# Kernel optimization log

Hardware: AMD Instinct MI355X
Metric: run time of the kernel (lower is better)

The kernel has to match this reference:

```python
import jax, jax.numpy as jnp
import numpy as np

EPS = 1e-07
CURVATURE = 1.0
MAX_NORM_RATIO = 0.99
B, L, N, K = 4, 2048, 2048, 2048


def _ternary_init(key, n, k):
    rand = jax.random.normal(key, (n, k), dtype=jnp.float32)
    threshold = 0.5 * jnp.mean(jnp.abs(rand))
    return jnp.where(rand > threshold, 1.0,
                     jnp.where(rand < -threshold, -1.0, 0.0)).astype(jnp.float32)


def setup_inputs() -> dict:
    key = jax.random.key(0)
    kx, kw = jax.random.split(key)
    x = jax.random.normal(kx, (B, L, N), dtype=jnp.float32)
    weight = _ternary_init(kw, N, K)  # ternary {-1,0,1} stored as fp32 (torch casts int8->float)
    scale = jnp.full((K,), 1.0 / np.sqrt(N), dtype=jnp.float32)
    return {"x": x, "weight": weight, "scale": scale}


def reference(x, weight, scale):
    sqrt_c = jnp.sqrt(jnp.float32(CURVATURE))
    # ternary matmul with per-output-column scale: (B,L,N)@(N,K) -> (B,L,K)
    out = jnp.einsum('bln,nk->blk', x, weight) * scale
    # Poincare exp map at origin: tanh(sqrt_c*|v|)/(sqrt_c*|v|) * v
    v_norm = jnp.maximum(jnp.linalg.norm(out, axis=-1, keepdims=True), EPS)
    scaled_norm = sqrt_c * v_norm
    out = out * (jnp.tanh(scaled_norm) / (scaled_norm + EPS))
    # normalize to ball: clamp norm to max_norm_ratio / sqrt(c)
    max_norm = MAX_NORM_RATIO / sqrt_c
    o_norm = jnp.maximum(jnp.linalg.norm(out, axis=-1, keepdims=True), EPS)
    out = out * jnp.minimum(max_norm / o_norm, 1.0)
    return out.astype(x.dtype)
```

## Files before the change

### kernel.cpp

```cpp
#include <hip/hip_runtime.h>
#include <hip/hip_bf16.h>
#include <stdint.h>
#include <math.h>

#define M_DIM 8192
#define K_DIM 2048
#define N_DIM 2048

#define BM 256
#define BN 256
#define BKB 128
#define NT (K_DIM / BKB)

typedef __attribute__((ext_vector_type(4))) int int32x4;
typedef __attribute__((ext_vector_type(16))) int int32x16;
typedef __attribute__((ext_vector_type(4))) float float4v;

__device__ __forceinline__ ushort f2bf(float f) {
    uint32_t u = __builtin_bit_cast(uint32_t, f);
    u = (u + 0x7fffu + ((u >> 16) & 1u)) >> 16;
    return (ushort)u;
}

#define GLD16(gp, lp)                                                          \
    __builtin_amdgcn_global_load_lds(                                          \
        (const __attribute__((address_space(1))) void*)(gp),                   \
        (__attribute__((address_space(3))) void*)(lp), 16, 0, 0)

#define BAR()                                                                  \
    do {                                                                       \
        asm volatile("" ::: "memory");                                         \
        __builtin_amdgcn_s_barrier();                                          \
        asm volatile("" ::: "memory");                                         \
    } while (0)

#define VMCNT(n) asm volatile("s_waitcnt vmcnt(" #n ")" ::: "memory")

__global__ __launch_bounds__(256) void transpose_w_i8(const float* __restrict__ W,
                                                      signed char* __restrict__ Wq) {
    __shared__ float tile[32][33];
    const int tb = blockIdx.x;
    const int kb = (tb & 63) * 32;
    const int nb = (tb >> 6) * 32;
    const int tx = threadIdx.x & 31;
    const int ty4 = (threadIdx.x >> 5) * 4;
#pragma unroll
    for (int i = 0; i < 4; i++)
        tile[ty4 + i][tx] = W[(size_t)(kb + ty4 + i) * N_DIM + nb + tx];
    __syncthreads();
    const int r = threadIdx.x >> 3;
    const int c4 = threadIdx.x & 7;
    uint32_t pk = 0;
#pragma unroll
    for (int j = 0; j < 4; j++) {
        const int q = (int)tile[c4 * 4 + j][r];
        pk |= (uint32_t)(q & 255) << (8 * j);
    }
    *(uint32_t*)&Wq[(size_t)(nb + r) * K_DIM + kb + c4 * 4] = pk;
}

__global__ __launch_bounds__(256) void quant_x(const float* __restrict__ X,
                                               signed char* __restrict__ Xq,
                                               float* __restrict__ srow) {
    const int row = blockIdx.x;
    const int t = threadIdx.x;
    const float* p = X + (size_t)row * K_DIM;
    float4v a = *(const float4v*)&p[t * 8];
    float4v b = *(const float4v*)&p[t * 8 + 4];
    float m = 0.f;
#pragma unroll
    for (int j = 0; j < 4; j++) m = fmaxf(m, fmaxf(fabsf(a[j]), fabsf(b[j])));
#pragma unroll
    for (int off = 1; off < 64; off <<= 1) m = fmaxf(m, __shfl_xor(m, off));
    __shared__ float wm[4];
    if ((t & 63) == 0) wm[t >> 6] = m;
    __syncthreads();
    float bm = fmaxf(fmaxf(wm[0], wm[1]), fmaxf(wm[2], wm[3]));
    bm = fmaxf(bm, 1e-8f);
    const float inv = 127.f / bm;
    uint32_t lo = 0, hi = 0;
#pragma unroll
    for (int j = 0; j < 4; j++) {
        const int qa = __float2int_rn(a[j] * inv);
        const int qb = __float2int_rn(b[j] * inv);
        lo |= (uint32_t)(qa & 255) << (8 * j);
        hi |= (uint32_t)(qb & 255) << (8 * j);
    }
    uint32_t* q = (uint32_t*)&Xq[(size_t)row * K_DIM + t * 8];
    q[0] = lo;
    q[1] = hi;
    if (t == 0) srow[row] = bm / 127.f;
}

__global__ __launch_bounds__(512, 1) void gemm_i8(const signed char* __restrict__ Xq,
                                                  const signed char* __restrict__ Wq,
                                                  const float* __restrict__ scale,
                                                  ushort* __restrict__ Cb) {
    __shared__ __align__(16) ushort lds[65536];

    const int tid = threadIdx.x;
    const int w = tid >> 6;
    const int lane = tid & 63;
    const int lrow = lane & 31;
    const int khalf = lane >> 5;
    const int rswz = lrow & 7;

    const int bid = blockIdx.x;
    const int wg = (bid & 7) * 32 + (bid >> 3);
    const int mt = wg >> 3;
    const int nt = wg & 7;
    const int row0 = mt * BM;
    const int col0 = nt * BN;

    const int wr = (w >> 2) * 128;
    const int wc = (w & 3) * 64;
    const int whalfA = w >> 2;
    const int whalfB = (w & 3) >> 1;
    const int wrB = (w & 1) * 64;

    int r_[2], c8_[2];
#pragma unroll
    for (int i = 0; i < 2; ++i) {
        const int q = (i * 8 + w) * 64 + lane;
        r_[i] = q >> 3;
        c8_[i] = (q & 7) ^ (r_[i] & 7);
    }

    auto stage2 = [&](const signed char* sb, int ldsbase) {
        GLD16(sb + (size_t)r_[0] * K_DIM + c8_[0] * 16, lds + ldsbase + (0 * 8 + w) * 512);
        GLD16(sb + (size_t)r_[1] * K_DIM + c8_[1] * 16, lds + ldsbase + (1 * 8 + w) * 512);
    };

#define RD_A(m, kk, base) (*(const int32x4*)&lds[(base) + ((m) * 32 + lrow) * 64 + ((((kk) * 2 + khalf) ^ rswz) * 8)])
#define RD_B(n, kk, base) (*(const int32x4*)&lds[(base) + (wrB + (n) * 32 + lrow) * 64 + ((((kk) * 2 + khalf) ^ rswz) * 8)])

    int32x16 acc[4][2] = {};

    const signed char* Asrc0 = Xq + (size_t)row0 * K_DIM;
    const signed char* Asrc1 = Xq + (size_t)(row0 + 128) * K_DIM;
    const signed char* Bsrc0 = Wq + (size_t)col0 * K_DIM;
    const signed char* Bsrc1 = Wq + (size_t)(col0 + 128) * K_DIM;

    stage2(Asrc0, 0 * 8192);
    stage2(Asrc1, 1 * 8192);
    stage2(Bsrc0, 32768 + 0 * 8192);
    stage2(Bsrc1, 32768 + 1 * 8192);
    VMCNT(0);
    BAR();

    for (int t = 0; t < NT; ++t) {
        const int abase = ((2 * t + whalfA) & 3) * 8192;
        const int bbase = 32768 + ((2 * t + whalfB) & 3) * 8192;
        const bool pf = (t + 1 < NT);
        const int aslot0 = ((2 * (t + 1)) & 3) * 8192;
        const int aslot1 = ((2 * (t + 1) + 1) & 3) * 8192;
        const int bslot0 = 32768 + ((2 * (t + 1)) & 3) * 8192;
        const int bslot1 = 32768 + ((2 * (t + 1) + 1) & 3) * 8192;

        if (pf) {
            stage2(Asrc0 + (t + 1) * BKB, aslot0);
            stage2(Asrc1 + (t + 1) * BKB, aslot1);
            stage2(Bsrc0 + (t + 1) * BKB, bslot0);
            stage2(Bsrc1 + (t + 1) * BKB, bslot1);
        }

#pragma unroll
        for (int kk = 0; kk < 4; ++kk) {
            int32x4 bfr[2], afr[4];
#pragma unroll
            for (int n = 0; n < 2; ++n) bfr[n] = RD_B(n, kk, bbase);
#pragma unroll
            for (int m = 0; m < 4; ++m) afr[m] = RD_A(m, kk, abase);
            __builtin_amdgcn_s_setprio(1);
#pragma unroll
            for (int m = 0; m < 4; ++m)
#pragma unroll
                for (int n = 0; n < 2; ++n)
                    acc[m][n] = __builtin_amdgcn_mfma_i32_32x32x32_i8(afr[m], bfr[n], acc[m][n], 0, 0, 0);
            __builtin_amdgcn_s_setprio(0);
        }

        VMCNT(0);
        BAR();
    }

    const int ccolb = col0 + wc + lrow;
    const int crowb = row0 + wr + 4 * khalf;
#pragma unroll
    for (int n = 0; n < 2; ++n) {
        const float sc = scale[ccolb + n * 32];
#pragma unroll
        for (int m = 0; m < 4; ++m) {
#pragma unroll
            for (int r = 0; r < 16; ++r) {
                const int row = crowb + m * 32 + (r & 3) + 8 * (r >> 2);
                const float v = (float)acc[m][n][r] * sc;
                Cb[(size_t)row * N_DIM + ccolb + n * 32] = f2bf(v);
            }
        }
    }
#undef RD_A
#undef RD_B
}

__global__ __launch_bounds__(256) void mobius_bf16(const ushort* __restrict__ Cb,
                                                   const float* __restrict__ srow,
                                                   float* __restrict__ out) {
    const int row = blockIdx.x;
    const ushort* p = Cb + (size_t)row * N_DIM;
    float* q = out + (size_t)row * N_DIM;
    const int t = threadIdx.x;
    const float s = srow[row];

    typedef __attribute__((ext_vector_type(8))) short short8;
    short8 v = *(const short8*)&p[t * 8];
    float f[8];
#pragma unroll
    for (int j = 0; j < 8; ++j) {
        const uint32_t u = ((uint32_t)(uint16_t)v[j]) << 16;
        f[j] = __builtin_bit_cast(float, u);
    }
    float ss = 0.f;
#pragma unroll
    for (int j = 0; j < 8; ++j) ss += f[j] * f[j];
#pragma unroll
    for (int off = 1; off < 64; off <<= 1) ss += __shfl_xor(ss, off);
    __shared__ float wsum[4];
    if ((t & 63) == 0) wsum[t >> 6] = ss;
    __syncthreads();
    const float tot = (wsum[0] + wsum[1] + wsum[2] + wsum[3]) * s * s;
    const float vn = fmaxf(sqrtf(tot), 1e-7f);
    const float tf = tanhf(vn) / (vn + 1e-7f);
    const float on = fmaxf(tf * vn, 1e-7f);
    const float g = s * tf * fminf(0.99f / on, 1.0f);
    float4v o0, o1;
#pragma unroll
    for (int j = 0; j < 4; ++j) { o0[j] = f[j] * g; o1[j] = f[4 + j] * g; }
    *(float4v*)&q[t * 8] = o0;
    *(float4v*)&q[t * 8 + 4] = o1;
}

extern "C" void kernel_launch(void* const* d_in, const int* in_sizes, int n_in,
                              void* d_out, int out_size, void* d_ws, size_t ws_size,
                              hipStream_t stream) {
    const float* x = (const float*)d_in[0];
    const float* w = (const float*)d_in[1];
    const float* scale = (const float*)d_in[2];
    float* out = (float*)d_out;

    signed char* Wq = (signed char*)d_ws;
    signed char* Xq = (signed char*)d_ws + 4194304;
    float* srow = (float*)((char*)d_ws + 20971520);
    ushort* Cb = (ushort*)((char*)d_ws + 21037056);

    transpose_w_i8<<<dim3(64 * 64), dim3(256), 0, stream>>>(w, Wq);
    quant_x<<<dim3(M_DIM), dim3(256), 0, stream>>>(x, Xq, srow);
    gemm_i8<<<dim3((M_DIM / BM) * (N_DIM / BN)), dim3(512), 0, stream>>>(Xq, Wq, scale, Cb);
    mobius_bf16<<<dim3(M_DIM), dim3(256), 0, stream>>>(Cb, srow, out);
}
```

Baseline: 81.22 us.

## Fuse Poincare row-norm epilogue into int8 GEMM via cross-block row reduction

Drops the separate mobius kernel and the bf16 intermediate buffer. Each GEMM block computes per-row partial sums of squares in LDS and writes them to a workspace. Blocks sharing a row tile then synchronize through an atomic counter spin-wait inside a cooperative launch, and each block scales its accumulators and writes fp32 output directly. This removes a full write and read of the bf16 intermediate plus one launch, at the cost of a spin barrier across the 8 column blocks, an extra memset, and uncoalesced scalar fp32 stores.

```diff
diff --git a/kernel.cpp b/kernel.cpp
--- a/kernel.cpp
+++ b/kernel.cpp
@@ -15,12 +15,6 @@
 typedef __attribute__((ext_vector_type(4))) int int32x4;
 typedef __attribute__((ext_vector_type(16))) int int32x16;
 typedef __attribute__((ext_vector_type(4))) float float4v;
-
-__device__ __forceinline__ ushort f2bf(float f) {
-    uint32_t u = __builtin_bit_cast(uint32_t, f);
-    u = (u + 0x7fffu + ((u >> 16) & 1u)) >> 16;
-    return (ushort)u;
-}
 
 #define GLD16(gp, lp)                                                          \
     __builtin_amdgcn_global_load_lds(                                          \
@@ -92,10 +86,13 @@
     if (t == 0) srow[row] = bm / 127.f;
 }
 
-__global__ __launch_bounds__(512, 1) void gemm_i8(const signed char* __restrict__ Xq,
-                                                  const signed char* __restrict__ Wq,
-                                                  const float* __restrict__ scale,
-                                                  ushort* __restrict__ Cb) {
+__global__ __launch_bounds__(512, 1) void gemm_i8_fused(const signed char* __restrict__ Xq,
+                                                        const signed char* __restrict__ Wq,
+                                                        const float* __restrict__ scale,
+                                                        const float* __restrict__ srow,
+                                                        float* __restrict__ out,
+                                                        float* __restrict__ wsp,
+                                                        int* __restrict__ cnt) {
     __shared__ __align__(16) ushort lds[65536];
 
     const int tid = threadIdx.x;
@@ -184,60 +181,69 @@
         BAR();
     }
 
+    float* lf = (float*)lds;
     const int ccolb = col0 + wc + lrow;
-    const int crowb = row0 + wr + 4 * khalf;
-#pragma unroll
-    for (int n = 0; n < 2; ++n) {
-        const float sc = scale[ccolb + n * 32];
-#pragma unroll
-        for (int m = 0; m < 4; ++m) {
-#pragma unroll
-            for (int r = 0; r < 16; ++r) {
-                const int row = crowb + m * 32 + (r & 3) + 8 * (r >> 2);
-                const float v = (float)acc[m][n][r] * sc;
-                Cb[(size_t)row * N_DIM + ccolb + n * 32] = f2bf(v);
-            }
+    const float sc0 = scale[ccolb];
+    const float sc1 = scale[ccolb + 32];
+    __syncthreads();
+
+#pragma unroll
+    for (int m = 0; m < 4; ++m) {
+#pragma unroll
+        for (int r = 0; r < 16; ++r) {
+            const int row_local = wr + 4 * khalf + m * 32 + (r & 3) + 8 * (r >> 2);
+            const float a0 = (float)acc[m][0][r] * sc0;
+            const float a1 = (float)acc[m][1][r] * sc1;
+            lf[row_local * 128 + (w & 3) * 32 + lrow] = a0 * a0 + a1 * a1;
+        }
+    }
+    __syncthreads();
+
+    if (tid < 256) {
+        float s = 0.f;
+        const int base = tid * 128;
+#pragma unroll 8
+        for (int e = 0; e < 128; ++e) s += lf[base + ((e + tid) & 127)];
+        __hip_atomic_store(&wsp[(size_t)(row0 + tid) * 8 + nt], s,
+                           __ATOMIC_RELAXED, __HIP_MEMORY_SCOPE_AGENT);
+    }
+    __syncthreads();
+
+    if (tid == 0) {
+        __hip_atomic_fetch_add(&cnt[mt], 1, __ATOMIC_ACQ_REL, __HIP_MEMORY_SCOPE_AGENT);
+        while (__hip_atomic_load(&cnt[mt], __ATOMIC_ACQUIRE, __HIP_MEMORY_SCOPE_AGENT) < 8)
+            __builtin_amdgcn_s_sleep(8);
+    }
+    __syncthreads();
+
+    if (tid < 256) {
+        float tot = 0.f;
+#pragma unroll
+        for (int j = 0; j < 8; ++j)
+            tot += __hip_atomic_load(&wsp[(size_t)(row0 + tid) * 8 + j],
+                                     __ATOMIC_RELAXED, __HIP_MEMORY_SCOPE_AGENT);
+        const float s = srow[row0 + tid];
+        tot *= s * s;
+        const float vn = fmaxf(sqrtf(tot), 1e-7f);
+        const float tf = tanhf(vn) / (vn + 1e-7f);
+        const float on = fmaxf(tf * vn, 1e-7f);
+        lf[tid] = s * tf * fminf(0.99f / on, 1.0f);
+    }
+    __syncthreads();
+
+#pragma unroll
+    for (int m = 0; m < 4; ++m) {
+#pragma unroll
+        for (int r = 0; r < 16; ++r) {
+            const int row_local = wr + 4 * khalf + m * 32 + (r & 3) + 8 * (r >> 2);
+            const float g = lf[row_local];
+            float* o = out + (size_t)(row0 + row_local) * N_DIM;
+            o[ccolb] = (float)acc[m][0][r] * sc0 * g;
+            o[ccolb + 32] = (float)acc[m][1][r] * sc1 * g;
         }
     }
 #undef RD_A
 #undef RD_B
-}
-
-__global__ __launch_bounds__(256) void mobius_bf16(const ushort* __restrict__ Cb,
-                                                   const float* __restrict__ srow,
-                                                   float* __restrict__ out) {
-    const int row = blockIdx.x;
-    const ushort* p = Cb + (size_t)row * N_DIM;
-    float* q = out + (size_t)row * N_DIM;
-    const int t = threadIdx.x;
-    const float s = srow[row];
-
-    typedef __attribute__((ext_vector_type(8))) short short8;
-    short8 v = *(const short8*)&p[t * 8];
-    float f[8];
-#pragma unroll
-    for (int j = 0; j < 8; ++j) {
-        const uint32_t u = ((uint32_t)(uint16_t)v[j]) << 16;
-        f[j] = __builtin_bit_cast(float, u);
-    }
-    float ss = 0.f;
-#pragma unroll
-    for (int j = 0; j < 8; ++j) ss += f[j] * f[j];
-#pragma unroll
-    for (int off = 1; off < 64; off <<= 1) ss += __shfl_xor(ss, off);
-    __shared__ float wsum[4];
-    if ((t & 63) == 0) wsum[t >> 6] = ss;
-    __syncthreads();
-    const float tot = (wsum[0] + wsum[1] + wsum[2] + wsum[3]) * s * s;
-    const float vn = fmaxf(sqrtf(tot), 1e-7f);
-    const float tf = tanhf(vn) / (vn + 1e-7f);
-    const float on = fmaxf(tf * vn, 1e-7f);
-    const float g = s * tf * fminf(0.99f / on, 1.0f);
-    float4v o0, o1;
-#pragma unroll
-    for (int j = 0; j < 4; ++j) { o0[j] = f[j] * g; o1[j] = f[4 + j] * g; }
-    *(float4v*)&q[t * 8] = o0;
-    *(float4v*)&q[t * 8 + 4] = o1;
 }
 
 extern "C" void kernel_launch(void* const* d_in, const int* in_sizes, int n_in,
@@ -251,10 +257,17 @@
     signed char* Wq = (signed char*)d_ws;
     signed char* Xq = (signed char*)d_ws + 4194304;
     float* srow = (float*)((char*)d_ws + 20971520);
-    ushort* Cb = (ushort*)((char*)d_ws + 21037056);
-
+    float* wsp = (float*)((char*)d_ws + 21037056);
+    int* cnt = (int*)((char*)d_ws + 21299200);
+
+    hipMemsetAsync(cnt, 0, 32 * sizeof(int), stream);
     transpose_w_i8<<<dim3(64 * 64), dim3(256), 0, stream>>>(w, Wq);
     quant_x<<<dim3(M_DIM), dim3(256), 0, stream>>>(x, Xq, srow);
-    gemm_i8<<<dim3((M_DIM / BM) * (N_DIM / BN)), dim3(512), 0, stream>>>(Xq, Wq, scale, Cb);
-    mobius_bf16<<<dim3(M_DIM), dim3(256), 0, stream>>>(Cb, srow, out);
-}
+
+    const signed char* XqC = Xq;
+    const signed char* WqC = Wq;
+    const float* srowC = srow;
+    void* args[] = {(void*)&XqC, (void*)&WqC, (void*)&scale, (void*)&srowC,
+                    (void*)&out, (void*)&wsp, (void*)&cnt};
+    hipLaunchCooperativeKernel((const void*)gemm_i8_fused, dim3(256), dim3(512), args, 0, stream);
+}
```

Result: slower. 107.4 us (+32.3%).

## Shrink GEMM tiles to 128x128 with 16x16x64 int8 MFMA and higher occupancy

Applied to the files above, without the earlier changes.

Restructures the int8 GEMM from 256x256 tiles with 512 threads and 32x32x32 MFMA to 128x128x64 tiles with 256 threads, 4 blocks per CU, and 16x16x64 MFMA. LDS shrinks to a simple double buffer with a new swizzle, and the epilogue mapping changes to match. The aim is more resident waves for latency hiding and a better-balanced grid. The cost is less data reuse per tile, so global and LDS traffic per FLOP goes up, plus more barriers per unit of work.

```diff
diff --git a/kernel.cpp b/kernel.cpp
--- a/kernel.cpp
+++ b/kernel.cpp
@@ -7,13 +7,12 @@
 #define K_DIM 2048
 #define N_DIM 2048
 
-#define BM 256
-#define BN 256
-#define BKB 128
+#define BM 128
+#define BN 128
+#define BKB 64
 #define NT (K_DIM / BKB)
 
 typedef __attribute__((ext_vector_type(4))) int int32x4;
-typedef __attribute__((ext_vector_type(16))) int int32x16;
 typedef __attribute__((ext_vector_type(4))) float float4v;
 
 __device__ __forceinline__ ushort f2bf(float f) {
@@ -92,115 +91,99 @@
     if (t == 0) srow[row] = bm / 127.f;
 }
 
-__global__ __launch_bounds__(512, 1) void gemm_i8(const signed char* __restrict__ Xq,
+__global__ __launch_bounds__(256, 4) void gemm_i8(const signed char* __restrict__ Xq,
                                                   const signed char* __restrict__ Wq,
                                                   const float* __restrict__ scale,
                                                   ushort* __restrict__ Cb) {
-    __shared__ __align__(16) ushort lds[65536];
+    __shared__ __align__(16) ushort lds[16384];
 
     const int tid = threadIdx.x;
     const int w = tid >> 6;
     const int lane = tid & 63;
-    const int lrow = lane & 31;
-    const int khalf = lane >> 5;
-    const int rswz = lrow & 7;
+    const int lrow = lane & 15;
+    const int khi3 = lane >> 4;
+    const int rswz = (lrow & 3) ^ (lrow >> 2);
 
     const int bid = blockIdx.x;
-    const int wg = (bid & 7) * 32 + (bid >> 3);
-    const int mt = wg >> 3;
-    const int nt = wg & 7;
+    const int wg = (bid & 7) * 128 + (bid >> 3);
+    const int mt = wg >> 4;
+    const int nt = wg & 15;
     const int row0 = mt * BM;
     const int col0 = nt * BN;
 
-    const int wr = (w >> 2) * 128;
-    const int wc = (w & 3) * 64;
-    const int whalfA = w >> 2;
-    const int whalfB = (w & 3) >> 1;
-    const int wrB = (w & 1) * 64;
-
-    int r_[2], c8_[2];
+    const int wr = (w >> 1) * 64;
+    const int wc = (w & 1) * 64;
+
+    int r_[2], cs_[2];
 #pragma unroll
     for (int i = 0; i < 2; ++i) {
-        const int q = (i * 8 + w) * 64 + lane;
-        r_[i] = q >> 3;
-        c8_[i] = (q & 7) ^ (r_[i] & 7);
-    }
-
-    auto stage2 = [&](const signed char* sb, int ldsbase) {
-        GLD16(sb + (size_t)r_[0] * K_DIM + c8_[0] * 16, lds + ldsbase + (0 * 8 + w) * 512);
-        GLD16(sb + (size_t)r_[1] * K_DIM + c8_[1] * 16, lds + ldsbase + (1 * 8 + w) * 512);
+        const int s = (i * 4 + w) * 64 + lane;
+        const int r = s >> 2;
+        r_[i] = r;
+        cs_[i] = (s & 3) ^ ((r & 3) ^ ((r >> 2) & 3));
+    }
+
+    auto stageM = [&](const signed char* srcbase, int kbyte, int ldsbase) {
+#pragma unroll
+        for (int i = 0; i < 2; ++i) {
+            GLD16(srcbase + (size_t)r_[i] * K_DIM + kbyte + cs_[i] * 16,
+                  lds + ldsbase + (i * 4 + w) * 512);
+        }
     };
 
-#define RD_A(m, kk, base) (*(const int32x4*)&lds[(base) + ((m) * 32 + lrow) * 64 + ((((kk) * 2 + khalf) ^ rswz) * 8)])
-#define RD_B(n, kk, base) (*(const int32x4*)&lds[(base) + (wrB + (n) * 32 + lrow) * 64 + ((((kk) * 2 + khalf) ^ rswz) * 8)])
-
-    int32x16 acc[4][2] = {};
-
-    const signed char* Asrc0 = Xq + (size_t)row0 * K_DIM;
-    const signed char* Asrc1 = Xq + (size_t)(row0 + 128) * K_DIM;
-    const signed char* Bsrc0 = Wq + (size_t)col0 * K_DIM;
-    const signed char* Bsrc1 = Wq + (size_t)(col0 + 128) * K_DIM;
-
-    stage2(Asrc0, 0 * 8192);
-    stage2(Asrc1, 1 * 8192);
-    stage2(Bsrc0, 32768 + 0 * 8192);
-    stage2(Bsrc1, 32768 + 1 * 8192);
+#define RD(base, q) (*(const int32x4*)&lds[(base) + ((q) * 16 + lrow) * 32 + ((khi3 ^ rswz) * 8)])
+
+    int32x4 acc[4][4] = {};
+
+    const signed char* Asrc = Xq + (size_t)row0 * K_DIM;
+    const signed char* Bsrc = Wq + (size_t)col0 * K_DIM;
+
+    stageM(Asrc, 0, 0);
+    stageM(Bsrc, 0, 8192);
     VMCNT(0);
     BAR();
 
     for (int t = 0; t < NT; ++t) {
-        const int abase = ((2 * t + whalfA) & 3) * 8192;
-        const int bbase = 32768 + ((2 * t + whalfB) & 3) * 8192;
-        const bool pf = (t + 1 < NT);
-        const int aslot0 = ((2 * (t + 1)) & 3) * 8192;
-        const int aslot1 = ((2 * (t + 1) + 1) & 3) * 8192;
-        const int bslot0 = 32768 + ((2 * (t + 1)) & 3) * 8192;
-        const int bslot1 = 32768 + ((2 * (t + 1) + 1) & 3) * 8192;
-
-        if (pf) {
-            stage2(Asrc0 + (t + 1) * BKB, aslot0);
-            stage2(Asrc1 + (t + 1) * BKB, aslot1);
-            stage2(Bsrc0 + (t + 1) * BKB, bslot0);
-            stage2(Bsrc1 + (t + 1) * BKB, bslot1);
+        const int abase = (t & 1) * 4096;
+        const int bbase = 8192 + (t & 1) * 4096;
+
+        if (t + 1 < NT) {
+            stageM(Asrc, (t + 1) * BKB, ((t + 1) & 1) * 4096);
+            stageM(Bsrc, (t + 1) * BKB, 8192 + ((t + 1) & 1) * 4096);
         }
 
-#pragma unroll
-        for (int kk = 0; kk < 4; ++kk) {
-            int32x4 bfr[2], afr[4];
-#pragma unroll
-            for (int n = 0; n < 2; ++n) bfr[n] = RD_B(n, kk, bbase);
-#pragma unroll
-            for (int m = 0; m < 4; ++m) afr[m] = RD_A(m, kk, abase);
-            __builtin_amdgcn_s_setprio(1);
-#pragma unroll
-            for (int m = 0; m < 4; ++m)
-#pragma unroll
-                for (int n = 0; n < 2; ++n)
-                    acc[m][n] = __builtin_amdgcn_mfma_i32_32x32x32_i8(afr[m], bfr[n], acc[m][n], 0, 0, 0);
-            __builtin_amdgcn_s_setprio(0);
-        }
+        int32x4 af[4], bf[4];
+#pragma unroll
+        for (int n = 0; n < 4; ++n) bf[n] = RD(bbase + wc * 32 / 16 * 16, n);
+#pragma unroll
+        for (int m = 0; m < 4; ++m) af[m] = RD(abase + wr * 32, m);
+        __builtin_amdgcn_s_setprio(1);
+#pragma unroll
+        for (int m = 0; m < 4; ++m)
+#pragma unroll
+            for (int n = 0; n < 4; ++n)
+                acc[m][n] = __builtin_amdgcn_mfma_i32_16x16x64_i8(af[m], bf[n], acc[m][n], 0, 0, 0);
+        __builtin_amdgcn_s_setprio(0);
 
         VMCNT(0);
         BAR();
     }
 
-    const int ccolb = col0 + wc + lrow;
-    const int crowb = row0 + wr + 4 * khalf;
-#pragma unroll
-    for (int n = 0; n < 2; ++n) {
-        const float sc = scale[ccolb + n * 32];
+    const int crow0 = row0 + wr + khi3 * 4;
+    const int ccol = col0 + wc + lrow;
+#pragma unroll
+    for (int n = 0; n < 4; ++n) {
+        const float sc = scale[ccol + n * 16];
 #pragma unroll
         for (int m = 0; m < 4; ++m) {
 #pragma unroll
-            for (int r = 0; r < 16; ++r) {
-                const int row = crowb + m * 32 + (r & 3) + 8 * (r >> 2);
-                const float v = (float)acc[m][n][r] * sc;
-                Cb[(size_t)row * N_DIM + ccolb + n * 32] = f2bf(v);
+            for (int j = 0; j < 4; ++j) {
+                const float v = (float)acc[m][n][j] * sc;
+                Cb[(size_t)(crow0 + m * 16 + j) * N_DIM + ccol + n * 16] = f2bf(v);
             }
         }
     }
-#undef RD_A
-#undef RD_B
+#undef RD
 }
 
 __global__ __launch_bounds__(256) void mobius_bf16(const ushort* __restrict__ Cb,
@@ -255,6 +238,6 @@
 
     transpose_w_i8<<<dim3(64 * 64), dim3(256), 0, stream>>>(w, Wq);
     quant_x<<<dim3(M_DIM), dim3(256), 0, stream>>>(x, Xq, srow);
-    gemm_i8<<<dim3((M_DIM / BM) * (N_DIM / BN)), dim3(512), 0, stream>>>(Xq, Wq, scale, Cb);
+    gemm_i8<<<dim3((M_DIM / BM) * (N_DIM / BN)), dim3(256), 0, stream>>>(Xq, Wq, scale, Cb);
     mobius_bf16<<<dim3(M_DIM), dim3(256), 0, stream>>>(Cb, srow, out);
 }
```

Measured after the change: 85.72 us. +5.5%, slower.

## Load B fragments directly to registers and triple-buffer A tiles in LDS

Applied to the files above, without the earlier changes.

The int8 GEMM no longer stages weight tiles through LDS. Each wave loads its B fragments from global memory straight into double-buffered registers, one tile ahead. A tiles move to a three-slot LDS ring prefetched two tiles ahead, with a partial vmcnt wait so loads overlap compute. This removes the LDS traffic and LDS footprint for B, at the cost of more registers and uncoalesced per-lane global loads of the weights, which are re-read by each wave.

```diff
diff --git a/kernel.cpp b/kernel.cpp
--- a/kernel.cpp
+++ b/kernel.cpp
@@ -96,7 +96,7 @@
                                                   const signed char* __restrict__ Wq,
                                                   const float* __restrict__ scale,
                                                   ushort* __restrict__ Cb) {
-    __shared__ __align__(16) ushort lds[65536];
+    __shared__ __align__(16) ushort lds[49152];
 
     const int tid = threadIdx.x;
     const int w = tid >> 6;
@@ -115,8 +115,6 @@
     const int wr = (w >> 2) * 128;
     const int wc = (w & 3) * 64;
     const int whalfA = w >> 2;
-    const int whalfB = (w & 3) >> 1;
-    const int wrB = (w & 1) * 64;
 
     int r_[2], c8_[2];
 #pragma unroll
@@ -126,63 +124,65 @@
         c8_[i] = (q & 7) ^ (r_[i] & 7);
     }
 
-    auto stage2 = [&](const signed char* sb, int ldsbase) {
-        GLD16(sb + (size_t)r_[0] * K_DIM + c8_[0] * 16, lds + ldsbase + (0 * 8 + w) * 512);
-        GLD16(sb + (size_t)r_[1] * K_DIM + c8_[1] * 16, lds + ldsbase + (1 * 8 + w) * 512);
-    };
-
-#define RD_A(m, kk, base) (*(const int32x4*)&lds[(base) + ((m) * 32 + lrow) * 64 + ((((kk) * 2 + khalf) ^ rswz) * 8)])
-#define RD_B(n, kk, base) (*(const int32x4*)&lds[(base) + (wrB + (n) * 32 + lrow) * 64 + ((((kk) * 2 + khalf) ^ rswz) * 8)])
-
-    int32x16 acc[4][2] = {};
-
     const signed char* Asrc0 = Xq + (size_t)row0 * K_DIM;
     const signed char* Asrc1 = Xq + (size_t)(row0 + 128) * K_DIM;
-    const signed char* Bsrc0 = Wq + (size_t)col0 * K_DIM;
-    const signed char* Bsrc1 = Wq + (size_t)(col0 + 128) * K_DIM;
-
-    stage2(Asrc0, 0 * 8192);
-    stage2(Asrc1, 1 * 8192);
-    stage2(Bsrc0, 32768 + 0 * 8192);
-    stage2(Bsrc1, 32768 + 1 * 8192);
-    VMCNT(0);
+
+    auto stageA = [&](int kbyte, int b) {
+        const int base = b * 16384;
+        GLD16(Asrc0 + (size_t)r_[0] * K_DIM + kbyte + c8_[0] * 16, lds + base + (0 * 8 + w) * 512);
+        GLD16(Asrc0 + (size_t)r_[1] * K_DIM + kbyte + c8_[1] * 16, lds + base + (1 * 8 + w) * 512);
+        GLD16(Asrc1 + (size_t)r_[0] * K_DIM + kbyte + c8_[0] * 16, lds + base + 8192 + (0 * 8 + w) * 512);
+        GLD16(Asrc1 + (size_t)r_[1] * K_DIM + kbyte + c8_[1] * 16, lds + base + 8192 + (1 * 8 + w) * 512);
+    };
+
+#define RD_A(m, kk, base) (*(const int32x4*)&lds[(base) + ((m) * 32 + lrow) * 64 + ((((kk) * 2 + khalf) ^ rswz) * 8)])
+
+    const signed char* Bp0 = Wq + (size_t)(col0 + wc + lrow) * K_DIM + khalf * 16;
+    const signed char* Bp1 = Bp0 + (size_t)32 * K_DIM;
+
+    int32x16 acc[4][2] = {};
+    int32x4 bE[2][4], bO[2][4];
+
+#pragma unroll
+    for (int kk = 0; kk < 4; ++kk) {
+        bE[0][kk] = *(const int32x4*)&Bp0[kk * 32];
+        bE[1][kk] = *(const int32x4*)&Bp1[kk * 32];
+    }
+    stageA(0, 0);
+    stageA(BKB, 1);
+    VMCNT(4);
     BAR();
 
-    for (int t = 0; t < NT; ++t) {
-        const int abase = ((2 * t + whalfA) & 3) * 8192;
-        const int bbase = 32768 + ((2 * t + whalfB) & 3) * 8192;
-        const bool pf = (t + 1 < NT);
-        const int aslot0 = ((2 * (t + 1)) & 3) * 8192;
-        const int aslot1 = ((2 * (t + 1) + 1) & 3) * 8192;
-        const int bslot0 = 32768 + ((2 * (t + 1)) & 3) * 8192;
-        const int bslot1 = 32768 + ((2 * (t + 1) + 1) & 3) * 8192;
-
-        if (pf) {
-            stage2(Asrc0 + (t + 1) * BKB, aslot0);
-            stage2(Asrc1 + (t + 1) * BKB, aslot1);
-            stage2(Bsrc0 + (t + 1) * BKB, bslot0);
-            stage2(Bsrc1 + (t + 1) * BKB, bslot1);
-        }
-
-#pragma unroll
-        for (int kk = 0; kk < 4; ++kk) {
-            int32x4 bfr[2], afr[4];
-#pragma unroll
-            for (int n = 0; n < 2; ++n) bfr[n] = RD_B(n, kk, bbase);
-#pragma unroll
-            for (int m = 0; m < 4; ++m) afr[m] = RD_A(m, kk, abase);
-            __builtin_amdgcn_s_setprio(1);
-#pragma unroll
-            for (int m = 0; m < 4; ++m)
-#pragma unroll
-                for (int n = 0; n < 2; ++n)
-                    acc[m][n] = __builtin_amdgcn_mfma_i32_32x32x32_i8(afr[m], bfr[n], acc[m][n], 0, 0, 0);
-            __builtin_amdgcn_s_setprio(0);
-        }
-
-        VMCNT(0);
-        BAR();
-    }
+#define TILE_BODY(T, CUR, NXT)                                                                     \
+    do {                                                                                           \
+        const int t_ = (T);                                                                        \
+        const int abase = (t_ % 3) * 16384 + whalfA * 8192;                                        \
+        if (t_ + 1 < NT) {                                                                         \
+            _Pragma("unroll") for (int kk = 0; kk < 4; ++kk) {                                     \
+                NXT[0][kk] = *(const int32x4*)&Bp0[(t_ + 1) * BKB + kk * 32];                      \
+                NXT[1][kk] = *(const int32x4*)&Bp1[(t_ + 1) * BKB + kk * 32];                      \
+            }                                                                                      \
+        }                                                                                          \
+        if (t_ + 2 < NT) stageA((t_ + 2) * BKB, (t_ + 2) % 3);                                     \
+        _Pragma("unroll") for (int kk = 0; kk < 4; ++kk) {                                         \
+            int32x4 af[4];                                                                         \
+            _Pragma("unroll") for (int m = 0; m < 4; ++m) af[m] = RD_A(m, kk, abase);              \
+            __builtin_amdgcn_s_setprio(1);                                                         \
+            _Pragma("unroll") for (int m = 0; m < 4; ++m) {                                        \
+                acc[m][0] = __builtin_amdgcn_mfma_i32_32x32x32_i8(af[m], CUR[0][kk], acc[m][0], 0, 0, 0); \
+                acc[m][1] = __builtin_amdgcn_mfma_i32_32x32x32_i8(af[m], CUR[1][kk], acc[m][1], 0, 0, 0); \
+            }                                                                                      \
+            __builtin_amdgcn_s_setprio(0);                                                         \
+        }                                                                                          \
+        if (t_ < NT - 2) { VMCNT(4); } else { VMCNT(0); }                                          \
+        BAR();                                                                                     \
+    } while (0)
+
+    for (int t = 0; t < NT; t += 2) {
+        TILE_BODY(t, bE, bO);
+        TILE_BODY(t + 1, bO, bE);
+    }
+#undef TILE_BODY
 
     const int ccolb = col0 + wc + lrow;
     const int crowb = row0 + wr + 4 * khalf;
@@ -200,7 +200,6 @@
         }
     }
 #undef RD_A
-#undef RD_B
 }
 
 __global__ __launch_bounds__(256) void mobius_bf16(const ushort* __restrict__ Cb,
```

New measurement: 94.15 us. 1.16x slower.
